# Performance work log

Measured on AMD Instinct MI355X. Metric: run time of the kernel, lower is better.

The kernel has to match this reference:

```python
import jax, jax.numpy as jnp
import numpy as np

NEG_INF = -1e9


def setup_inputs() -> dict:
    key = jax.random.key(0)
    ks = jax.random.split(key, 7)
    N, Q, C = 16, 4096, 77
    D, Dc, H, S = 512, 768, 8, 64
    scale = 0.02
    return {
        "query": jax.random.normal(ks[0], (N, Q, D), jnp.float32),
        "context": jax.random.normal(ks[1], (N, C, Dc), jnp.float32),
        "Wq": jax.random.normal(ks[2], (D, H, S), jnp.float32) * scale,
        "Wk": jax.random.normal(ks[3], (Dc, H, S), jnp.float32) * scale,
        "Wv": jax.random.normal(ks[4], (Dc, H, S), jnp.float32) * scale,
        "Wo": jax.random.normal(ks[5], (H, S, D), jnp.float32) * scale,
        "bo": jnp.zeros((D,), jnp.float32),
    }


def reference(query, context, Wq, Wk, Wv, Wo, bo):
    # Projections: split hidden dim into heads.
    q = jnp.einsum('NQD,DHS->NQHS', query, Wq)      # [N,Q,H,S]
    k = jnp.einsum('NCD,DHS->NCHS', context, Wk)    # [N,C,H,S]
    v = jnp.einsum('NCD,DHS->NCHS', context, Wv)    # [N,C,H,S]
    size_per_head = q.shape[-1]
    # Attention scores [N,H,Q,C], scaled by 1/sqrt(S).
    scores = jnp.einsum('NQHS,NCHS->NHQC', q, k) * (size_per_head ** -0.5)
    weights = jax.nn.softmax(scores, axis=3)
    out = jnp.einsum('NHQC,NCHS->NQHS', weights, v)  # [N,Q,H,S]
    # Merge heads back to model dim with output bias.
    return jnp.einsum('NQHS,HSD->NQD', out, Wo) + bo
```

## Files before the change

### kernel.cpp

```cpp
#include <hip/hip_runtime.h>

typedef unsigned short u16;
typedef unsigned int u32;
typedef __bf16 bf16_t;
typedef bf16_t bf16x8 __attribute__((ext_vector_type(8)));
typedef float floatx4 __attribute__((ext_vector_type(4)));

__device__ __forceinline__ float bf2f(u16 h) {
    union { unsigned u; float f; } v;
    v.u = ((unsigned)h) << 16;
    return v.f;
}

__device__ __forceinline__ u16 f2bf(float f) {
    union { float f; unsigned u; } v;
    v.f = f;
    unsigned r = v.u + 0x7fffu + ((v.u >> 16) & 1u);
    return (u16)(r >> 16);
}

typedef __attribute__((address_space(1))) const u32 gu32;
typedef __attribute__((address_space(3))) u32 lu32;
__device__ __forceinline__ void gload16(const void* g, void* l) {
    __builtin_amdgcn_global_load_lds((gu32*)g, (lu32*)l, 16, 0, 0);
}

__global__ void transpose_one(const float* __restrict__ W, u16* __restrict__ Wt,
                              int K, int N) {
    int idx = blockIdx.x * 256 + threadIdx.x;
    if (idx >= K * N) return;
    int nrow = idx / K;
    int k = idx - nrow * K;
    Wt[idx] = f2bf(W[k * N + nrow]);
}

__global__ void transpose_kv(const float* __restrict__ Wk, const float* __restrict__ Wv,
                             u16* __restrict__ Wt) {
    int idx = blockIdx.x * 256 + threadIdx.x;
    if (idx >= 1024 * 768) return;
    int nrow = idx / 768;
    int k = idx - nrow * 768;
    Wt[idx] = f2bf((nrow < 512) ? Wk[k * 512 + nrow] : Wv[k * 512 + (nrow - 512)]);
}

#define TM 128
#define TN 128
#define TK 32

template <bool A_F32, bool OUT_F32>
__global__ __launch_bounds__(256) void gemm_bt(
    const void* __restrict__ A_, const u16* __restrict__ Bt,
    void* __restrict__ C_, const float* __restrict__ bias,
    int M, int K, int N, int ntl2)
{
    constexpr int ABYTES = A_F32 ? TM * TK * 4 : TM * TK * 2;
    __shared__ __align__(16) char smem[ABYTES + TN * TK * 2];
    float* Asf = (float*)smem;
    u16*   Asb = (u16*)smem;
    u16*   Bs  = (u16*)(smem + ABYTES);

    const int tid  = threadIdx.x;
    const int lane = tid & 63;
    const int wave = tid >> 6;
    const int quad = lane >> 4;
    const int l16  = lane & 15;
    const int wm   = (wave & 1) * 64;
    const int wn   = (wave >> 1) * 64;

    const int nwg = gridDim.x;
    const int wg  = blockIdx.x;
    const int t   = (wg & 7) * (nwg >> 3) + (wg >> 3);
    const long bm = (long)(t >> ntl2) * TM;
    const long bn = (long)(t & ((1 << ntl2) - 1)) * TN;

    const float* Af = (const float*)A_;
    const u16*   Ab = (const u16*)A_;

    floatx4 acc[4][4] = {};

    for (int k0 = 0; k0 < K; k0 += TK) {
        #pragma unroll
        for (int p = 0; p < 2; ++p) {
            int ch  = p * 256 + tid;
            int row = ch >> 2;
            int pc  = ch & 3;
            gload16(Bt + (bn + row) * K + k0 + pc * 8,
                    Bs + (p * 256 + wave * 64) * 8);
        }
        if (A_F32) {
            #pragma unroll
            for (int p = 0; p < 4; ++p) {
                int ch  = p * 256 + tid;
                int row = ch >> 3;
                int pc  = ch & 7;
                long gr = bm + row;
                if (gr < M)
                    gload16(Af + gr * K + k0 + pc * 4,
                            Asf + (p * 256 + wave * 64) * 4);
            }
        } else {
            #pragma unroll
            for (int p = 0; p < 2; ++p) {
                int ch  = p * 256 + tid;
                int row = ch >> 2;
                int pc  = ch & 3;
                long gr = bm + row;
                if (gr < M)
                    gload16(Ab + gr * K + k0 + pc * 8,
                            Asb + (p * 256 + wave * 64) * 8);
            }
        }
        __syncthreads();

        bf16x8 af[4], bfr[4];
        #pragma unroll
        for (int i = 0; i < 4; ++i) {
            int row = wm + i * 16 + l16;
            if (A_F32) {
                const float* ap = Asf + row * 32 + quad * 8;
                float4 f0 = *(const float4*)ap;
                float4 f1 = *(const float4*)(ap + 4);
                union { u16 h[8]; bf16x8 v; } pk;
                pk.h[0] = f2bf(f0.x); pk.h[1] = f2bf(f0.y);
                pk.h[2] = f2bf(f0.z); pk.h[3] = f2bf(f0.w);
                pk.h[4] = f2bf(f1.x); pk.h[5] = f2bf(f1.y);
                pk.h[6] = f2bf(f1.z); pk.h[7] = f2bf(f1.w);
                af[i] = pk.v;
            } else {
                af[i] = *(const bf16x8*)(Asb + row * 32 + quad * 8);
            }
        }
        #pragma unroll
        for (int j = 0; j < 4; ++j)
            bfr[j] = *(const bf16x8*)(Bs + (wn + j * 16 + l16) * 32 + quad * 8);
        #pragma unroll
        for (int i = 0; i < 4; ++i)
            #pragma unroll
            for (int j = 0; j < 4; ++j)
                acc[i][j] = __builtin_amdgcn_mfma_f32_16x16x32_bf16(
                    af[i], bfr[j], acc[i][j], 0, 0, 0);
        __syncthreads();
    }

    #pragma unroll
    for (int i = 0; i < 4; ++i) {
        #pragma unroll
        for (int r = 0; r < 4; ++r) {
            long row = bm + wm + i * 16 + quad * 4 + r;
            if (row >= M) continue;
            #pragma unroll
            for (int j = 0; j < 4; ++j) {
                long col = bn + wn + j * 16 + l16;
                float val = acc[i][j][r];
                if (bias) val += bias[col];
                if (OUT_F32) ((float*)C_)[row * N + col] = val;
                else         ((u16*)C_)[row * N + col] = f2bf(val);
            }
        }
    }
}

__global__ __launch_bounds__(256) void attn_kernel(
    const u16* __restrict__ qb,
    const u16* __restrict__ kvb,
    u16* __restrict__ ob)
{
    const int QL = 4096, HS = 512;
    const int q0 = blockIdx.x * 256;
    const int h  = blockIdx.y;
    const int n  = blockIdx.z;

    __shared__ u16 sQP[128 * 104];
    __shared__ u16 ks [80 * 72];
    __shared__ u16 vts[64 * 104];

    const int tid  = threadIdx.x;
    const int lane = tid & 63;
    const int wave = tid >> 6;
    const int quad = lane >> 4;
    const int l16  = lane & 15;
    const int wm   = wave * 32;

    const u16* kbase = kvb + (long)n * 77 * 1024 + h * 64;
    for (int v = tid; v < 640; v += 256) {
        int c = v >> 3, g = (v & 7) * 8;
        uint4 val = make_uint4(0, 0, 0, 0);
        if (c < 77) val = *(const uint4*)(kbase + (long)c * 1024 + g);
        *(uint4*)(&ks[c * 72 + g]) = val;
    }
    const u16* vbase = kvb + (long)n * 77 * 1024 + 512 + h * 64;
    for (int v = tid; v < 616; v += 256) {
        int c = v >> 3, g = (v & 7) * 8;
        *(uint4*)(&sQP[c * 64 + g]) = *(const uint4*)(vbase + (long)c * 1024 + g);
    }
    __syncthreads();
    for (int e = tid; e < 64 * 96; e += 256) {
        int c = e >> 6, s = e & 63;
        u16 val = (c < 77) ? sQP[c * 64 + s] : (u16)0;
        vts[s * 104 + c] = val;
    }
    __syncthreads();

    const bool v4ok = (l16 < 13);

    for (int it = 0; it < 2; ++it) {
        const long qrow0 = (long)q0 + it * 128;
        const u16* qbase = qb + ((long)n * QL + qrow0) * HS + h * 64;
        u16*       obase = ob + ((long)n * QL + qrow0) * HS + h * 64;

        #pragma unroll
        for (int p = 0; p < 4; ++p) {
            int v = tid + p * 256;
            int r = v >> 3, g = (v & 7) * 8;
            *(uint4*)(&sQP[r * 72 + g]) = *(const uint4*)(qbase + (long)r * HS + g);
        }
        __syncthreads();

        floatx4 accS[2][5] = {};
        #pragma unroll
        for (int kk = 0; kk < 2; ++kk) {
            bf16x8 aq[2], bk[5];
            #pragma unroll
            for (int t = 0; t < 2; ++t)
                aq[t] = *(const bf16x8*)(&sQP[(wm + t * 16 + l16) * 72 + kk * 32 + quad * 8]);
            #pragma unroll
            for (int j = 0; j < 5; ++j)
                bk[j] = *(const bf16x8*)(&ks[(j * 16 + l16) * 72 + kk * 32 + quad * 8]);
            #pragma unroll
            for (int t = 0; t < 2; ++t)
                #pragma unroll
                for (int j = 0; j < 5; ++j)
                    accS[t][j] = __builtin_amdgcn_mfma_f32_16x16x32_bf16(
                        aq[t], bk[j], accS[t][j], 0, 0, 0);
        }

        float pw[2][5][4];
        #pragma unroll
        for (int t = 0; t < 2; ++t) {
            #pragma unroll
            for (int r = 0; r < 4; ++r) {
                float v0 = accS[t][0][r] * 0.125f;
                float v1 = accS[t][1][r] * 0.125f;
                float v2 = accS[t][2][r] * 0.125f;
                float v3 = accS[t][3][r] * 0.125f;
                float v4 = v4ok ? accS[t][4][r] * 0.125f : -1e30f;
                float mx = fmaxf(fmaxf(fmaxf(v0, v1), fmaxf(v2, v3)), v4);
                mx = fmaxf(mx, __shfl_xor(mx, 1));
                mx = fmaxf(mx, __shfl_xor(mx, 2));
                mx = fmaxf(mx, __shfl_xor(mx, 4));
                mx = fmaxf(mx, __shfl_xor(mx, 8));
                float e0 = __expf(v0 - mx), e1 = __expf(v1 - mx);
                float e2 = __expf(v2 - mx), e3 = __expf(v3 - mx);
                float e4 = __expf(v4 - mx);
                float sum = e0 + e1 + e2 + e3 + e4;
                sum += __shfl_xor(sum, 1);
                sum += __shfl_xor(sum, 2);
                sum += __shfl_xor(sum, 4);
                sum += __shfl_xor(sum, 8);
                float inv = 1.f / sum;
                pw[t][0][r] = e0 * inv; pw[t][1][r] = e1 * inv;
                pw[t][2][r] = e2 * inv; pw[t][3][r] = e3 * inv;
                pw[t][4][r] = e4 * inv;
            }
        }
        __syncthreads();

        #pragma unroll
        for (int t = 0; t < 2; ++t) {
            #pragma unroll
            for (int r = 0; r < 4; ++r) {
                int row = wm + t * 16 + quad * 4 + r;
                #pragma unroll
                for (int j = 0; j < 5; ++j)
                    sQP[row * 104 + j * 16 + l16] = f2bf(pw[t][j][r]);
                sQP[row * 104 + 80 + l16] = 0;
            }
        }
        __syncthreads();

        floatx4 accO[2][4] = {};
        #pragma unroll
        for (int kk = 0; kk < 3; ++kk) {
            bf16x8 aw[2], bv[4];
            #pragma unroll
            for (int t = 0; t < 2; ++t)
                aw[t] = *(const bf16x8*)(&sQP[(wm + t * 16 + l16) * 104 + kk * 32 + quad * 8]);
            #pragma unroll
            for (int j = 0; j < 4; ++j)
                bv[j] = *(const bf16x8*)(&vts[(j * 16 + l16) * 104 + kk * 32 + quad * 8]);
            #pragma unroll
            for (int t = 0; t < 2; ++t)
                #pragma unroll
                for (int j = 0; j < 4; ++j)
                    accO[t][j] = __builtin_amdgcn_mfma_f32_16x16x32_bf16(
                        aw[t], bv[j], accO[t][j], 0, 0, 0);
        }

        #pragma unroll
        for (int t = 0; t < 2; ++t)
            #pragma unroll
            for (int j = 0; j < 4; ++j)
                #pragma unroll
                for (int r = 0; r < 4; ++r) {
                    int row = wm + t * 16 + quad * 4 + r;
                    obase[(long)row * HS + j * 16 + l16] = f2bf(accO[t][j][r]);
                }
        __syncthreads();
    }
}

extern "C" void kernel_launch(void* const* d_in, const int* in_sizes, int n_in,
                              void* d_out, int out_size, void* d_ws, size_t ws_size,
                              hipStream_t stream) {
    const float* query   = (const float*)d_in[0];
    const float* context = (const float*)d_in[1];
    const float* Wq      = (const float*)d_in[2];
    const float* Wk      = (const float*)d_in[3];
    const float* Wv      = (const float*)d_in[4];
    const float* Wo      = (const float*)d_in[5];
    const float* bo      = (const float*)d_in[6];
    float* out = (float*)d_out;

    u16* q_ws  = (u16*)d_ws;
    u16* kv_ws = q_ws + 33554432;
    u16* WqT   = kv_ws + 1261568;
    u16* WkvT  = WqT + 262144;
    u16* WoT   = WkvT + 786432;

    transpose_one<<<(512 * 512 + 255) / 256, 256, 0, stream>>>(Wq, WqT, 512, 512);
    transpose_kv<<<(1024 * 768 + 255) / 256, 256, 0, stream>>>(Wk, Wv, WkvT);
    transpose_one<<<(512 * 512 + 255) / 256, 256, 0, stream>>>(Wo, WoT, 512, 512);

    gemm_bt<true, false><<<dim3(2048), 256, 0, stream>>>(
        (const void*)query, WqT, (void*)q_ws, nullptr, 65536, 512, 512, 2);
    gemm_bt<true, false><<<dim3(80), 256, 0, stream>>>(
        (const void*)context, WkvT, (void*)kv_ws, nullptr, 1232, 768, 1024, 3);
    attn_kernel<<<dim3(16, 8, 16), 256, 0, stream>>>(q_ws, kv_ws, q_ws);
    gemm_bt<false, true><<<dim3(2048), 256, 0, stream>>>(
        (const void*)q_ws, WoT, (void*)out, bo, 65536, 512, 512, 2);
}
```

Measured before the change: 451.9 us.

## Double-buffer GEMM LDS tiles, swizzle A tile, pretranspose V in separate kernel

The GEMM main loop now keeps two LDS stages and issues the next tile's global-to-LDS loads before computing the current one, so load latency overlaps with MFMA work. The fp32 A tile is stored with an XOR swizzle to cut LDS bank conflicts, and the manual bf16 rounding is replaced by native bf16 casts. A new kernel pretransposes V into a padded per-head layout, so the attention kernel loads it directly instead of doing its own LDS transpose. The cost is double the LDS per block, which can lower occupancy, plus one extra launch. The transposed V reuses the WkvT weight buffer after the KV GEMM has finished with it.

```diff
diff --git a/kernel.cpp b/kernel.cpp
--- a/kernel.cpp
+++ b/kernel.cpp
@@ -43,6 +43,20 @@
     Wt[idx] = f2bf((nrow < 512) ? Wk[k * 512 + nrow] : Wv[k * 512 + (nrow - 512)]);
 }
 
+__global__ void transpose_v(const u16* __restrict__ kv, u16* __restrict__ vt) {
+    int idx = blockIdx.x * 256 + threadIdx.x;
+    if (idx >= 16 * 8 * 64 * 96) return;
+    int c  = idx % 96;
+    int t1 = idx / 96;
+    int s  = t1 & 63;
+    int t2 = t1 >> 6;
+    int h  = t2 & 7;
+    int n  = t2 >> 3;
+    u16 val = 0;
+    if (c < 77) val = kv[((long)(n * 77 + c)) * 1024 + 512 + h * 64 + s];
+    vt[idx] = val;
+}
+
 #define TM 128
 #define TN 128
 #define TK 32
@@ -53,11 +67,9 @@
     void* __restrict__ C_, const float* __restrict__ bias,
     int M, int K, int N, int ntl2)
 {
-    constexpr int ABYTES = A_F32 ? TM * TK * 4 : TM * TK * 2;
-    __shared__ __align__(16) char smem[ABYTES + TN * TK * 2];
-    float* Asf = (float*)smem;
-    u16*   Asb = (u16*)smem;
-    u16*   Bs  = (u16*)(smem + ABYTES);
+    constexpr int AB = A_F32 ? TM * TK * 4 : TM * TK * 2;
+    constexpr int BB = TN * TK * 2;
+    __shared__ __align__(16) char smem[2 * (AB + BB)];
 
     const int tid  = threadIdx.x;
     const int lane = tid & 63;
@@ -78,25 +90,27 @@
 
     floatx4 acc[4][4] = {};
 
-    for (int k0 = 0; k0 < K; k0 += TK) {
+    auto stage = [&](int b, int k0) {
+        char* Abase = smem + b * (AB + BB);
+        u16*  Bb    = (u16*)(Abase + AB);
         #pragma unroll
         for (int p = 0; p < 2; ++p) {
             int ch  = p * 256 + tid;
             int row = ch >> 2;
             int pc  = ch & 3;
             gload16(Bt + (bn + row) * K + k0 + pc * 8,
-                    Bs + (p * 256 + wave * 64) * 8);
+                    Bb + (p * 256 + wave * 64) * 8);
         }
         if (A_F32) {
             #pragma unroll
             for (int p = 0; p < 4; ++p) {
                 int ch  = p * 256 + tid;
                 int row = ch >> 3;
-                int pc  = ch & 7;
+                int pcs = (ch & 7) ^ (row & 7);
                 long gr = bm + row;
                 if (gr < M)
-                    gload16(Af + gr * K + k0 + pc * 4,
-                            Asf + (p * 256 + wave * 64) * 4);
+                    gload16(Af + gr * K + k0 + pcs * 4,
+                            (float*)Abase + (p * 256 + wave * 64) * 4);
             }
         } else {
             #pragma unroll
@@ -107,38 +121,51 @@
                 long gr = bm + row;
                 if (gr < M)
                     gload16(Ab + gr * K + k0 + pc * 8,
-                            Asb + (p * 256 + wave * 64) * 8);
-            }
-        }
-        __syncthreads();
+                            (u16*)Abase + (p * 256 + wave * 64) * 8);
+            }
+        }
+    };
+
+    const int nk = K / TK;
+    stage(0, 0);
+    __syncthreads();
+
+    for (int tt = 0; tt < nk; ++tt) {
+        const int cb = tt & 1;
+        if (tt + 1 < nk) stage(cb ^ 1, (tt + 1) * TK);
+
+        const char* Abase = smem + cb * (AB + BB);
+        const u16*  Bb    = (const u16*)(Abase + AB);
 
         bf16x8 af[4], bfr[4];
         #pragma unroll
         for (int i = 0; i < 4; ++i) {
             int row = wm + i * 16 + l16;
             if (A_F32) {
-                const float* ap = Asf + row * 32 + quad * 8;
-                float4 f0 = *(const float4*)ap;
-                float4 f1 = *(const float4*)(ap + 4);
-                union { u16 h[8]; bf16x8 v; } pk;
-                pk.h[0] = f2bf(f0.x); pk.h[1] = f2bf(f0.y);
-                pk.h[2] = f2bf(f0.z); pk.h[3] = f2bf(f0.w);
-                pk.h[4] = f2bf(f1.x); pk.h[5] = f2bf(f1.y);
-                pk.h[6] = f2bf(f1.z); pk.h[7] = f2bf(f1.w);
+                const char* arow = Abase + (size_t)row * 128;
+                int x = row & 7;
+                float4 f0 = *(const float4*)(arow + (((quad * 2)     ^ x) * 16));
+                float4 f1 = *(const float4*)(arow + (((quad * 2 + 1) ^ x) * 16));
+                union { bf16_t h[8]; bf16x8 v; } pk;
+                pk.h[0] = (bf16_t)f0.x; pk.h[1] = (bf16_t)f0.y;
+                pk.h[2] = (bf16_t)f0.z; pk.h[3] = (bf16_t)f0.w;
+                pk.h[4] = (bf16_t)f1.x; pk.h[5] = (bf16_t)f1.y;
+                pk.h[6] = (bf16_t)f1.z; pk.h[7] = (bf16_t)f1.w;
                 af[i] = pk.v;
             } else {
-                af[i] = *(const bf16x8*)(Asb + row * 32 + quad * 8);
+                af[i] = *(const bf16x8*)((const u16*)Abase + row * 32 + quad * 8);
             }
         }
         #pragma unroll
         for (int j = 0; j < 4; ++j)
-            bfr[j] = *(const bf16x8*)(Bs + (wn + j * 16 + l16) * 32 + quad * 8);
+            bfr[j] = *(const bf16x8*)(Bb + (wn + j * 16 + l16) * 32 + quad * 8);
         #pragma unroll
         for (int i = 0; i < 4; ++i)
             #pragma unroll
             for (int j = 0; j < 4; ++j)
                 acc[i][j] = __builtin_amdgcn_mfma_f32_16x16x32_bf16(
                     af[i], bfr[j], acc[i][j], 0, 0, 0);
+
         __syncthreads();
     }
 
@@ -163,6 +190,7 @@
 __global__ __launch_bounds__(256) void attn_kernel(
     const u16* __restrict__ qb,
     const u16* __restrict__ kvb,
+    const u16* __restrict__ vt,
     u16* __restrict__ ob)
 {
     const int QL = 4096, HS = 512;
@@ -188,16 +216,10 @@
         if (c < 77) val = *(const uint4*)(kbase + (long)c * 1024 + g);
         *(uint4*)(&ks[c * 72 + g]) = val;
     }
-    const u16* vbase = kvb + (long)n * 77 * 1024 + 512 + h * 64;
-    for (int v = tid; v < 616; v += 256) {
-        int c = v >> 3, g = (v & 7) * 8;
-        *(uint4*)(&sQP[c * 64 + g]) = *(const uint4*)(vbase + (long)c * 1024 + g);
-    }
-    __syncthreads();
-    for (int e = tid; e < 64 * 96; e += 256) {
-        int c = e >> 6, s = e & 63;
-        u16 val = (c < 77) ? sQP[c * 64 + s] : (u16)0;
-        vts[s * 104 + c] = val;
+    const u16* vtbase = vt + (long)((n * 8 + h) * 64) * 96;
+    for (int v = tid; v < 768; v += 256) {
+        int r = v / 12, c8 = v - r * 12;
+        *(uint4*)(&vts[r * 104 + c8 * 8]) = *(const uint4*)(vtbase + v * 8);
     }
     __syncthreads();
 
@@ -326,6 +348,7 @@
     u16* WqT   = kv_ws + 1261568;
     u16* WkvT  = WqT + 262144;
     u16* WoT   = WkvT + 786432;
+    u16* vt_ws = WkvT;
 
     transpose_one<<<(512 * 512 + 255) / 256, 256, 0, stream>>>(Wq, WqT, 512, 512);
     transpose_kv<<<(1024 * 768 + 255) / 256, 256, 0, stream>>>(Wk, Wv, WkvT);
@@ -335,7 +358,8 @@
         (const void*)query, WqT, (void*)q_ws, nullptr, 65536, 512, 512, 2);
     gemm_bt<true, false><<<dim3(80), 256, 0, stream>>>(
         (const void*)context, WkvT, (void*)kv_ws, nullptr, 1232, 768, 1024, 3);
-    attn_kernel<<<dim3(16, 8, 16), 256, 0, stream>>>(q_ws, kv_ws, q_ws);
+    transpose_v<<<(16 * 8 * 64 * 96 + 255) / 256, 256, 0, stream>>>(kv_ws, vt_ws);
+    attn_kernel<<<dim3(16, 8, 16), 256, 0, stream>>>(q_ws, kv_ws, vt_ws, q_ws);
     gemm_bt<false, true><<<dim3(2048), 256, 0, stream>>>(
         (const void*)q_ws, WoT, (void*)out, bo, 65536, 512, 512, 2);
 }
```

After: 444.6 us. Within noise of the previous version (-1.6%).
